# Kernel optimization log

Measured on AMD Instinct MI355X. Metric: run time of the kernel, lower is better.

The kernel has to match this reference:

```python
import jax, jax.numpy as jnp
import numpy as np

N, D, H, O, E, K = 8192, 1024, 4096, 1024, 8, 3  # tokens, in_dim, hidden, out_dim, experts, topk


def setup_inputs() -> dict:
    key = jax.random.key(0)
    ks = jax.random.split(key, 4)
    s = 0.02
    return {
        "x": jax.random.normal(ks[0], (N, D), jnp.float32),
        "gate_w": jax.random.normal(ks[1], (D, E), jnp.float32) * s,
        "gate_b": jnp.zeros((E,), jnp.float32),
        "w1": jax.random.normal(ks[2], (E, D, H), jnp.float32) * s,
        "b1": jnp.zeros((E, H), jnp.float32),
        "w2": jax.random.normal(ks[3], (E, H, O), jnp.float32) * s,
        "b2": jnp.zeros((E, O), jnp.float32),
    }


def reference(x, gate_w, gate_b, w1, b1, w2, b2):
    # Gate: scores over experts, top-k mask, softmax renormalized over selected experts
    scores = x @ gate_w + gate_b                                   # [N, E]
    _, topk_idx = jax.lax.top_k(scores, K)                         # [N, K]
    mask = jax.nn.one_hot(topk_idx, E, dtype=scores.dtype).sum(1)  # [N, E] (topk indices are distinct)
    weights = jax.nn.softmax(scores, axis=-1) * mask
    weights = weights / (weights.sum(-1, keepdims=True) + 1e-8)
    # Dense all-expert MLP (faithful to original: every expert runs on every token)
    h = jax.nn.relu(jnp.einsum('nd,edh->neh', x, w1) + b1)         # [N, E, H]
    outs = jnp.einsum('neh,eho->neo', h, w2) + b2                  # [N, E, O]
    # Weighted combine over experts
    return jnp.einsum('ne,neo->no', weights, outs)                 # [N, O]
```

## Files before the change

kernel.cpp:

```cpp
#include <hip/hip_runtime.h>
#include <hip/hip_bf16.h>
#include <hip/hip_fp16.h>

#define N_TOK 8192
#define DIM_D 1024
#define DIM_H 4096
#define DIM_O 1024
#define NEXP  8
#define TOPK  3

#define CAP_ROWS  25600
#define MAX_TILES 200

typedef _Float16 f16_t;
typedef _Float16 f16x4 __attribute__((ext_vector_type(4)));
typedef _Float16 f16x8 __attribute__((ext_vector_type(8)));
typedef float    floatx4 __attribute__((ext_vector_type(4)));

__device__ __forceinline__ void gld_lds16(const void* g, void* l) {
  __builtin_amdgcn_global_load_lds(
      (__attribute__((address_space(1))) void*)(void*)g,
      (__attribute__((address_space(3))) void*)l, 16, 0, 0);
}

__global__ __launch_bounds__(256) void gate_kernel(
    const float* __restrict__ x, const float* __restrict__ gw,
    const float* __restrict__ gb, float* __restrict__ wts,
    int* __restrict__ lists, int* __restrict__ cnt) {
  const int token = blockIdx.x * 4 + (threadIdx.x >> 6);
  const int lane = threadIdx.x & 63;
  float s[NEXP];
#pragma unroll
  for (int e = 0; e < NEXP; e++) s[e] = 0.f;
  const float* xr = x + (size_t)token * DIM_D;
  for (int d = lane; d < DIM_D; d += 64) {
    const float xv = xr[d];
    const float* g = gw + (size_t)d * NEXP;
#pragma unroll
    for (int e = 0; e < NEXP; e++) s[e] += xv * g[e];
  }
#pragma unroll
  for (int off = 32; off > 0; off >>= 1) {
#pragma unroll
    for (int e = 0; e < NEXP; e++) s[e] += __shfl_xor(s[e], off, 64);
  }
#pragma unroll
  for (int e = 0; e < NEXP; e++) s[e] += gb[e];

  float mx = s[0];
#pragma unroll
  for (int e = 1; e < NEXP; e++) mx = fmaxf(mx, s[e]);
  float p[NEXP];
  float den = 0.f;
#pragma unroll
  for (int e = 0; e < NEXP; e++) { p[e] = expf(s[e] - mx); den += p[e]; }

  bool sel[NEXP];
#pragma unroll
  for (int e = 0; e < NEXP; e++) sel[e] = false;
  for (int k = 0; k < TOPK; k++) {
    int bj = 0;
    float bv = -1e30f;
#pragma unroll
    for (int e = 0; e < NEXP; e++) {
      if (!sel[e] && s[e] > bv) { bv = s[e]; bj = e; }
    }
    sel[bj] = true;
  }
  float msum = 1e-8f * den;
#pragma unroll
  for (int e = 0; e < NEXP; e++) msum += sel[e] ? p[e] : 0.f;
  const float inv = 1.f / msum;
  if (lane < NEXP) {
    wts[(size_t)token * NEXP + lane] = sel[lane] ? p[lane] * inv : 0.f;
  }
  if (lane == 0) {
#pragma unroll
    for (int e = 0; e < NEXP; e++) {
      if (sel[e]) {
        const int pos = atomicAdd(&cnt[e], 1);
        lists[e * N_TOK + pos] = token;
      }
    }
  }
}

__global__ void plan_kernel(const int* __restrict__ cnt, int* __restrict__ start,
                            int* __restrict__ table, int* __restrict__ total) {
  if (threadIdx.x == 0) {
    int r0 = 0, t = 0;
    for (int e = 0; e < NEXP; e++) {
      start[e] = r0;
      const int nt = (cnt[e] + 127) >> 7;
      for (int i = 0; i < nt; i++) table[t++] = (e << 16) | ((r0 >> 7) + i);
      r0 += nt << 7;
    }
    total[0] = t;
  }
}

__global__ __launch_bounds__(256) void fill_kernel(
    const int* __restrict__ cnt, const int* __restrict__ start,
    const int* __restrict__ lists, const float* __restrict__ wts,
    int* __restrict__ rowtok, float* __restrict__ roww) {
  const int e = blockIdx.y;
  const int i = blockIdx.x * 256 + threadIdx.x;
  const int c = cnt[e];
  const int pad = (c + 127) & ~127;
  if (i >= pad) return;
  const int r = start[e] + i;
  if (i < c) {
    const int t = lists[e * N_TOK + i];
    rowtok[r] = t;
    roww[r] = wts[(size_t)t * NEXP + e];
  } else {
    rowtok[r] = -1;
    roww[r] = 0.f;
  }
}

__global__ __launch_bounds__(256) void cvt_f32_f16(
    const float* __restrict__ in, f16_t* __restrict__ out, int n4) {
  const int i = blockIdx.x * 256 + threadIdx.x;
  if (i >= n4) return;
  const float4 v = ((const float4*)in)[i];
  f16x4 o;
  o.x = (f16_t)v.x; o.y = (f16_t)v.y; o.z = (f16_t)v.z; o.w = (f16_t)v.w;
  ((f16x4*)out)[i] = o;
}

__global__ __launch_bounds__(256) void cvt_transpose(
    const float* __restrict__ in, f16_t* __restrict__ out, int R, int C) {
  __shared__ float tile[32][33];
  const int e = blockIdx.z;
  const int r0 = blockIdx.y * 32, c0 = blockIdx.x * 32;
  const int lc = threadIdx.x & 31, lr0 = threadIdx.x >> 5;
  const float* src = in + (size_t)e * R * C;
#pragma unroll
  for (int i = 0; i < 4; i++) {
    const int rr = lr0 + i * 8;
    tile[rr][lc] = src[(size_t)(r0 + rr) * C + c0 + lc];
  }
  __syncthreads();
  f16_t* dst = out + (size_t)e * C * R;
#pragma unroll
  for (int i = 0; i < 4; i++) {
    const int cc = lr0 + i * 8;
    dst[(size_t)(c0 + cc) * R + r0 + lc] = (f16_t)tile[lc][cc];
  }
}

__global__ __launch_bounds__(256, 2) void gemm1_moe(
    const f16_t* __restrict__ xb, const f16_t* __restrict__ w1t,
    const float* __restrict__ b1, const int* __restrict__ rowtok,
    const int* __restrict__ table, const int* __restrict__ total,
    f16_t* __restrict__ hg, int Hc, int cH) {
  const int mt = blockIdx.y;
  if (mt >= total[0]) return;
  const int ent = table[mt];
  const int e = ent >> 16;
  const int r0 = (ent & 0xffff) << 7;
  const int n0 = blockIdx.x * 128;

  __shared__ __align__(16) f16_t Asm[128 * 32];
  __shared__ __align__(16) f16_t Bsm[128 * 32];
  const int tid = threadIdx.x;
  const int wave = tid >> 6, lane = tid & 63;
  const int q = lane >> 4, r = lane & 15;
  const int waveM = (wave >> 1) * 64, waveN = (wave & 1) * 64;

  const floatx4 zero = {0.f, 0.f, 0.f, 0.f};
  floatx4 acc[4][4];
#pragma unroll
  for (int mi = 0; mi < 4; mi++)
#pragma unroll
    for (int ni = 0; ni < 4; ni++) acc[mi][ni] = zero;

  const f16_t* BT = w1t + (size_t)e * DIM_H * DIM_D + (size_t)cH * DIM_D;

  const int s0 = tid, s1 = tid + 256;
  const int row0 = s0 >> 2, row1 = s1 >> 2;
  const int gs0 = (s0 & 3) ^ ((row0 >> 1) & 3);
  const int gs1 = (s1 & 3) ^ ((row1 >> 1) & 3);
  const int tok0 = max(rowtok[r0 + row0], 0);
  const int tok1 = max(rowtok[r0 + row1], 0);
  const f16_t* Ar0 = xb + (size_t)tok0 * DIM_D + gs0 * 8;
  const f16_t* Ar1 = xb + (size_t)tok1 * DIM_D + gs1 * 8;
  const f16_t* Br0 = BT + (size_t)(n0 + row0) * DIM_D + gs0 * 8;
  const f16_t* Br1 = BT + (size_t)(n0 + row1) * DIM_D + gs1 * 8;
  f16_t* AsmB0 = &Asm[(wave * 64) * 8];
  f16_t* AsmB1 = &Asm[(256 + wave * 64) * 8];
  f16_t* BsmB0 = &Bsm[(wave * 64) * 8];
  f16_t* BsmB1 = &Bsm[(256 + wave * 64) * 8];

  for (int k0 = 0; k0 < DIM_D; k0 += 32) {
    gld_lds16(Ar0 + k0, AsmB0);
    gld_lds16(Ar1 + k0, AsmB1);
    gld_lds16(Br0 + k0, BsmB0);
    gld_lds16(Br1 + k0, BsmB1);
    __syncthreads();
    f16x8 af[4], bfr[4];
#pragma unroll
    for (int i = 0; i < 4; i++) {
      const int rowa = waveM + i * 16 + r;
      af[i] = *(const f16x8*)&Asm[rowa * 32 + ((q ^ ((rowa >> 1) & 3)) << 3)];
      const int rowb = waveN + i * 16 + r;
      bfr[i] = *(const f16x8*)&Bsm[rowb * 32 + ((q ^ ((rowb >> 1) & 3)) << 3)];
    }
#pragma unroll
    for (int mi = 0; mi < 4; mi++)
#pragma unroll
      for (int ni = 0; ni < 4; ni++)
        acc[mi][ni] = __builtin_amdgcn_mfma_f32_16x16x32_f16(
            af[mi], bfr[ni], acc[mi][ni], 0, 0, 0);
    __syncthreads();
  }

#pragma unroll
  for (int mi = 0; mi < 4; mi++)
#pragma unroll
    for (int ni = 0; ni < 4; ni++) {
      const int gcol = n0 + waveN + ni * 16 + r;
      const float bv = b1[(size_t)e * DIM_H + cH + gcol];
#pragma unroll
      for (int rr = 0; rr < 4; rr++) {
        const int grow = r0 + waveM + mi * 16 + q * 4 + rr;
        hg[(size_t)grow * Hc + gcol] = (f16_t)fmaxf(acc[mi][ni][rr] + bv, 0.f);
      }
    }
}

__global__ __launch_bounds__(256, 2) void gemm2_moe(
    const f16_t* __restrict__ hg, const f16_t* __restrict__ w2t,
    const float* __restrict__ b2, const int* __restrict__ rowtok,
    const float* __restrict__ roww, const int* __restrict__ table,
    const int* __restrict__ total, float* __restrict__ out, int Hc, int cH,
    int addBias) {
  const int mt = blockIdx.y;
  if (mt >= total[0]) return;
  const int ent = table[mt];
  const int e = ent >> 16;
  const int r0 = (ent & 0xffff) << 7;
  const int n0 = blockIdx.x * 128;

  __shared__ __align__(16) f16_t Asm[128 * 32];
  __shared__ __align__(16) f16_t Bsm[128 * 32];
  const int tid = threadIdx.x;
  const int wave = tid >> 6, lane = tid & 63;
  const int q = lane >> 4, r = lane & 15;
  const int waveM = (wave >> 1) * 64, waveN = (wave & 1) * 64;

  const floatx4 zero = {0.f, 0.f, 0.f, 0.f};
  floatx4 acc[4][4];
#pragma unroll
  for (int mi = 0; mi < 4; mi++)
#pragma unroll
    for (int ni = 0; ni < 4; ni++) acc[mi][ni] = zero;

  const f16_t* BT = w2t + (size_t)e * DIM_O * DIM_H + cH;

  const int s0 = tid, s1 = tid + 256;
  const int row0 = s0 >> 2, row1 = s1 >> 2;
  const int gs0 = (s0 & 3) ^ ((row0 >> 1) & 3);
  const int gs1 = (s1 & 3) ^ ((row1 >> 1) & 3);
  const f16_t* Ar0 = hg + (size_t)(r0 + row0) * Hc + gs0 * 8;
  const f16_t* Ar1 = hg + (size_t)(r0 + row1) * Hc + gs1 * 8;
  const f16_t* Br0 = BT + (size_t)(n0 + row0) * DIM_H + gs0 * 8;
  const f16_t* Br1 = BT + (size_t)(n0 + row1) * DIM_H + gs1 * 8;
  f16_t* AsmB0 = &Asm[(wave * 64) * 8];
  f16_t* AsmB1 = &Asm[(256 + wave * 64) * 8];
  f16_t* BsmB0 = &Bsm[(wave * 64) * 8];
  f16_t* BsmB1 = &Bsm[(256 + wave * 64) * 8];

  for (int k0 = 0; k0 < Hc; k0 += 32) {
    gld_lds16(Ar0 + k0, AsmB0);
    gld_lds16(Ar1 + k0, AsmB1);
    gld_lds16(Br0 + k0, BsmB0);
    gld_lds16(Br1 + k0, BsmB1);
    __syncthreads();
    f16x8 af[4], bfr[4];
#pragma unroll
    for (int i = 0; i < 4; i++) {
      const int rowa = waveM + i * 16 + r;
      af[i] = *(const f16x8*)&Asm[rowa * 32 + ((q ^ ((rowa >> 1) & 3)) << 3)];
      const int rowb = waveN + i * 16 + r;
      bfr[i] = *(const f16x8*)&Bsm[rowb * 32 + ((q ^ ((rowb >> 1) & 3)) << 3)];
    }
#pragma unroll
    for (int mi = 0; mi < 4; mi++)
#pragma unroll
      for (int ni = 0; ni < 4; ni++)
        acc[mi][ni] = __builtin_amdgcn_mfma_f32_16x16x32_f16(
            af[mi], bfr[ni], acc[mi][ni], 0, 0, 0);
    __syncthreads();
  }

#pragma unroll
  for (int mi = 0; mi < 4; mi++)
#pragma unroll
    for (int ni = 0; ni < 4; ni++) {
      const int gcol = n0 + waveN + ni * 16 + r;
      const float bv = addBias ? b2[(size_t)e * DIM_O + gcol] : 0.f;
#pragma unroll
      for (int rr = 0; rr < 4; rr++) {
        const int grow = r0 + waveM + mi * 16 + q * 4 + rr;
        const int t = rowtok[grow];
        if (t >= 0) {
          const float w = roww[grow];
          unsafeAtomicAdd(&out[(size_t)t * DIM_O + gcol],
                          w * (acc[mi][ni][rr] + bv));
        }
      }
    }
}

extern "C" void kernel_launch(void* const* d_in, const int* in_sizes, int n_in,
                              void* d_out, int out_size, void* d_ws, size_t ws_size,
                              hipStream_t stream) {
  const float* x      = (const float*)d_in[0];
  const float* gate_w = (const float*)d_in[1];
  const float* gate_b = (const float*)d_in[2];
  const float* w1     = (const float*)d_in[3];
  const float* b1     = (const float*)d_in[4];
  const float* w2     = (const float*)d_in[5];
  const float* b2     = (const float*)d_in[6];
  float* out = (float*)d_out;

  char* ws = (char*)d_ws;
  const size_t off_wts    = 0;
  const size_t off_lists  = off_wts + 262144;
  const size_t off_cnt    = off_lists + 262144;
  const size_t off_start  = off_cnt + 512;
  const size_t off_total  = off_start + 512;
  const size_t off_table  = off_total + 512;
  const size_t off_rowtok = off_table + 2048;
  const size_t off_roww   = off_rowtok + 102400;
  const size_t META       = 1 << 20;
  const size_t off_w1t = META;
  const size_t off_w2t = off_w1t + (size_t)NEXP * DIM_H * DIM_D * 2;
  const size_t off_xb  = off_w2t + (size_t)NEXP * DIM_O * DIM_H * 2;
  const size_t off_hg  = off_xb + (size_t)N_TOK * DIM_D * 2;

  float* wts   = (float*)(ws + off_wts);
  int*   lists = (int*)(ws + off_lists);
  int*   cnt   = (int*)(ws + off_cnt);
  int*   start = (int*)(ws + off_start);
  int*   total = (int*)(ws + off_total);
  int*   table = (int*)(ws + off_table);
  int*   rowtok= (int*)(ws + off_rowtok);
  float* roww  = (float*)(ws + off_roww);
  f16_t* w1t   = (f16_t*)(ws + off_w1t);
  f16_t* w2t   = (f16_t*)(ws + off_w2t);
  f16_t* xb    = (f16_t*)(ws + off_xb);
  f16_t* hg    = (f16_t*)(ws + off_hg);

  int Hc = 512;
  for (int cand = 4096; cand >= 512; cand >>= 1) {
    if (off_hg + (size_t)CAP_ROWS * cand * 2 <= ws_size) { Hc = cand; break; }
  }
  const int nchunks = DIM_H / Hc;

  hipMemsetAsync(cnt, 0, 512, stream);
  hipMemsetAsync(d_out, 0, (size_t)out_size * sizeof(float), stream);

  gate_kernel<<<N_TOK / 4, 256, 0, stream>>>(x, gate_w, gate_b, wts, lists, cnt);
  plan_kernel<<<1, 64, 0, stream>>>(cnt, start, table, total);
  fill_kernel<<<dim3(N_TOK / 256, NEXP), 256, 0, stream>>>(
      cnt, start, lists, wts, rowtok, roww);

  const int n4 = N_TOK * DIM_D / 4;
  cvt_f32_f16<<<(n4 + 255) / 256, 256, 0, stream>>>(x, xb, n4);
  cvt_transpose<<<dim3(DIM_H / 32, DIM_D / 32, NEXP), 256, 0, stream>>>(
      w1, w1t, DIM_D, DIM_H);
  cvt_transpose<<<dim3(DIM_O / 32, DIM_H / 32, NEXP), 256, 0, stream>>>(
      w2, w2t, DIM_H, DIM_O);

  for (int c = 0; c < nchunks; c++) {
    const int cH = c * Hc;
    gemm1_moe<<<dim3(Hc / 128, MAX_TILES), 256, 0, stream>>>(
        xb, w1t, b1, rowtok, table, total, hg, Hc, cH);
    gemm2_moe<<<dim3(DIM_O / 128, MAX_TILES), 256, 0, stream>>>(
        hg, w2t, b2, rowtok, roww, table, total, out, Hc, cH, c == 0);
  }
}
```

Measured before the change: 1.284 ms.

## Enlarge MoE GEMM row tiles to 256 and parallelize tile table construction

The grouped GEMM kernels now process 256-row tiles instead of 128, with each wave owning a 128x64 sub-tile and holding 8x4 MFMA accumulators. This doubles reuse of each B-operand load per LDS stage and halves the tile count. Expert row padding, capacity and workspace offsets are adjusted to match, and the plan kernel fills the tile table across threads. The larger tiles raise register pressure, which can lower occupancy, and add more padding waste per expert.

```diff
diff --git a/kernel.cpp b/kernel.cpp
--- a/kernel.cpp
+++ b/kernel.cpp
@@ -9,8 +9,8 @@
 #define NEXP  8
 #define TOPK  3
 
-#define CAP_ROWS  25600
-#define MAX_TILES 200
+#define CAP_ROWS  26624
+#define MAX_TILES 104
 
 typedef _Float16 f16_t;
 typedef _Float16 f16x4 __attribute__((ext_vector_type(4)));
@@ -85,17 +85,29 @@
   }
 }
 
-__global__ void plan_kernel(const int* __restrict__ cnt, int* __restrict__ start,
-                            int* __restrict__ table, int* __restrict__ total) {
+__global__ __launch_bounds__(256) void plan_kernel(
+    const int* __restrict__ cnt, int* __restrict__ start,
+    int* __restrict__ table, int* __restrict__ total) {
+  __shared__ int s_start[NEXP], s_tp[NEXP + 1];
   if (threadIdx.x == 0) {
     int r0 = 0, t = 0;
     for (int e = 0; e < NEXP; e++) {
-      start[e] = r0;
-      const int nt = (cnt[e] + 127) >> 7;
-      for (int i = 0; i < nt; i++) table[t++] = (e << 16) | ((r0 >> 7) + i);
-      r0 += nt << 7;
-    }
+      s_start[e] = r0;
+      s_tp[e] = t;
+      const int nt = (cnt[e] + 255) >> 8;
+      t += nt;
+      r0 += nt << 8;
+      start[e] = s_start[e];
+    }
+    s_tp[NEXP] = t;
     total[0] = t;
+  }
+  __syncthreads();
+  const int t = threadIdx.x;
+  if (t < s_tp[NEXP]) {
+    int e = 0;
+    while (t >= s_tp[e + 1]) e++;
+    table[t] = (e << 16) | ((s_start[e] >> 8) + (t - s_tp[e]));
   }
 }
 
@@ -106,7 +118,7 @@
   const int e = blockIdx.y;
   const int i = blockIdx.x * 256 + threadIdx.x;
   const int c = cnt[e];
-  const int pad = (c + 127) & ~127;
+  const int pad = (c + 255) & ~255;
   if (i >= pad) return;
   const int r = start[e] + i;
   if (i < c) {
@@ -159,56 +171,66 @@
   if (mt >= total[0]) return;
   const int ent = table[mt];
   const int e = ent >> 16;
-  const int r0 = (ent & 0xffff) << 7;
+  const int r0 = (ent & 0xffff) << 8;
   const int n0 = blockIdx.x * 128;
 
-  __shared__ __align__(16) f16_t Asm[128 * 32];
+  __shared__ __align__(16) f16_t Asm[256 * 32];
   __shared__ __align__(16) f16_t Bsm[128 * 32];
   const int tid = threadIdx.x;
   const int wave = tid >> 6, lane = tid & 63;
   const int q = lane >> 4, r = lane & 15;
-  const int waveM = (wave >> 1) * 64, waveN = (wave & 1) * 64;
+  const int waveM = (wave >> 1) * 128, waveN = (wave & 1) * 64;
 
   const floatx4 zero = {0.f, 0.f, 0.f, 0.f};
-  floatx4 acc[4][4];
-#pragma unroll
-  for (int mi = 0; mi < 4; mi++)
+  floatx4 acc[8][4];
+#pragma unroll
+  for (int mi = 0; mi < 8; mi++)
 #pragma unroll
     for (int ni = 0; ni < 4; ni++) acc[mi][ni] = zero;
 
   const f16_t* BT = w1t + (size_t)e * DIM_H * DIM_D + (size_t)cH * DIM_D;
 
-  const int s0 = tid, s1 = tid + 256;
-  const int row0 = s0 >> 2, row1 = s1 >> 2;
-  const int gs0 = (s0 & 3) ^ ((row0 >> 1) & 3);
-  const int gs1 = (s1 & 3) ^ ((row1 >> 1) & 3);
-  const int tok0 = max(rowtok[r0 + row0], 0);
-  const int tok1 = max(rowtok[r0 + row1], 0);
-  const f16_t* Ar0 = xb + (size_t)tok0 * DIM_D + gs0 * 8;
-  const f16_t* Ar1 = xb + (size_t)tok1 * DIM_D + gs1 * 8;
-  const f16_t* Br0 = BT + (size_t)(n0 + row0) * DIM_D + gs0 * 8;
-  const f16_t* Br1 = BT + (size_t)(n0 + row1) * DIM_D + gs1 * 8;
-  f16_t* AsmB0 = &Asm[(wave * 64) * 8];
-  f16_t* AsmB1 = &Asm[(256 + wave * 64) * 8];
-  f16_t* BsmB0 = &Bsm[(wave * 64) * 8];
-  f16_t* BsmB1 = &Bsm[(256 + wave * 64) * 8];
+  const f16_t* Asrc[4];
+  f16_t* AsmB[4];
+#pragma unroll
+  for (int j = 0; j < 4; j++) {
+    const int s = tid + j * 256;
+    const int row = s >> 2;
+    const int gs = (s & 3) ^ ((row >> 1) & 3);
+    const int tok = max(rowtok[r0 + row], 0);
+    Asrc[j] = xb + (size_t)tok * DIM_D + gs * 8;
+    AsmB[j] = &Asm[(wave * 64 + j * 256) * 8];
+  }
+  const f16_t* Bsrc[2];
+  f16_t* BsmB[2];
+#pragma unroll
+  for (int j = 0; j < 2; j++) {
+    const int s = tid + j * 256;
+    const int row = s >> 2;
+    const int gs = (s & 3) ^ ((row >> 1) & 3);
+    Bsrc[j] = BT + (size_t)(n0 + row) * DIM_D + gs * 8;
+    BsmB[j] = &Bsm[(wave * 64 + j * 256) * 8];
+  }
 
   for (int k0 = 0; k0 < DIM_D; k0 += 32) {
-    gld_lds16(Ar0 + k0, AsmB0);
-    gld_lds16(Ar1 + k0, AsmB1);
-    gld_lds16(Br0 + k0, BsmB0);
-    gld_lds16(Br1 + k0, BsmB1);
+#pragma unroll
+    for (int j = 0; j < 4; j++) gld_lds16(Asrc[j] + k0, AsmB[j]);
+#pragma unroll
+    for (int j = 0; j < 2; j++) gld_lds16(Bsrc[j] + k0, BsmB[j]);
     __syncthreads();
-    f16x8 af[4], bfr[4];
-#pragma unroll
-    for (int i = 0; i < 4; i++) {
+    f16x8 af[8], bfr[4];
+#pragma unroll
+    for (int i = 0; i < 8; i++) {
       const int rowa = waveM + i * 16 + r;
       af[i] = *(const f16x8*)&Asm[rowa * 32 + ((q ^ ((rowa >> 1) & 3)) << 3)];
+    }
+#pragma unroll
+    for (int i = 0; i < 4; i++) {
       const int rowb = waveN + i * 16 + r;
       bfr[i] = *(const f16x8*)&Bsm[rowb * 32 + ((q ^ ((rowb >> 1) & 3)) << 3)];
     }
 #pragma unroll
-    for (int mi = 0; mi < 4; mi++)
+    for (int mi = 0; mi < 8; mi++)
 #pragma unroll
       for (int ni = 0; ni < 4; ni++)
         acc[mi][ni] = __builtin_amdgcn_mfma_f32_16x16x32_f16(
@@ -217,7 +239,7 @@
   }
 
 #pragma unroll
-  for (int mi = 0; mi < 4; mi++)
+  for (int mi = 0; mi < 8; mi++)
 #pragma unroll
     for (int ni = 0; ni < 4; ni++) {
       const int gcol = n0 + waveN + ni * 16 + r;
@@ -240,54 +262,65 @@
   if (mt >= total[0]) return;
   const int ent = table[mt];
   const int e = ent >> 16;
-  const int r0 = (ent & 0xffff) << 7;
+  const int r0 = (ent & 0xffff) << 8;
   const int n0 = blockIdx.x * 128;
 
-  __shared__ __align__(16) f16_t Asm[128 * 32];
+  __shared__ __align__(16) f16_t Asm[256 * 32];
   __shared__ __align__(16) f16_t Bsm[128 * 32];
   const int tid = threadIdx.x;
   const int wave = tid >> 6, lane = tid & 63;
   const int q = lane >> 4, r = lane & 15;
-  const int waveM = (wave >> 1) * 64, waveN = (wave & 1) * 64;
+  const int waveM = (wave >> 1) * 128, waveN = (wave & 1) * 64;
 
   const floatx4 zero = {0.f, 0.f, 0.f, 0.f};
-  floatx4 acc[4][4];
-#pragma unroll
-  for (int mi = 0; mi < 4; mi++)
+  floatx4 acc[8][4];
+#pragma unroll
+  for (int mi = 0; mi < 8; mi++)
 #pragma unroll
     for (int ni = 0; ni < 4; ni++) acc[mi][ni] = zero;
 
   const f16_t* BT = w2t + (size_t)e * DIM_O * DIM_H + cH;
 
-  const int s0 = tid, s1 = tid + 256;
-  const int row0 = s0 >> 2, row1 = s1 >> 2;
-  const int gs0 = (s0 & 3) ^ ((row0 >> 1) & 3);
-  const int gs1 = (s1 & 3) ^ ((row1 >> 1) & 3);
-  const f16_t* Ar0 = hg + (size_t)(r0 + row0) * Hc + gs0 * 8;
-  const f16_t* Ar1 = hg + (size_t)(r0 + row1) * Hc + gs1 * 8;
-  const f16_t* Br0 = BT + (size_t)(n0 + row0) * DIM_H + gs0 * 8;
-  const f16_t* Br1 = BT + (size_t)(n0 + row1) * DIM_H + gs1 * 8;
-  f16_t* AsmB0 = &Asm[(wave * 64) * 8];
-  f16_t* AsmB1 = &Asm[(256 + wave * 64) * 8];
-  f16_t* BsmB0 = &Bsm[(wave * 64) * 8];
-  f16_t* BsmB1 = &Bsm[(256 + wave * 64) * 8];
+  const f16_t* Asrc[4];
+  f16_t* AsmB[4];
+#pragma unroll
+  for (int j = 0; j < 4; j++) {
+    const int s = tid + j * 256;
+    const int row = s >> 2;
+    const int gs = (s & 3) ^ ((row >> 1) & 3);
+    Asrc[j] = hg + (size_t)(r0 + row) * Hc + gs * 8;
+    AsmB[j] = &Asm[(wave * 64 + j * 256) * 8];
+  }
+  const f16_t* Bsrc[2];
+  f16_t* BsmB[2];
+#pragma unroll
+  for (int j = 0; j < 2; j++) {
+    const int s = tid + j * 256;
+    const int row = s >> 2;
+    const int gs = (s & 3) ^ ((row >> 1) & 3);
+    Bsrc[j] = BT + (size_t)(n0 + row) * DIM_H + gs * 8;
+    BsmB[j] = &Bsm[(wave * 64 + j * 256) * 8];
+  }
 
   for (int k0 = 0; k0 < Hc; k0 += 32) {
-    gld_lds16(Ar0 + k0, AsmB0);
-    gld_lds16(Ar1 + k0, AsmB1);
-    gld_lds16(Br0 + k0, BsmB0);
-    gld_lds16(Br1 + k0, BsmB1);
+#pragma unroll
+    for (int j = 0; j < 4; j++) gld_lds16(Asrc[j] + k0, AsmB[j]);
+#pragma unroll
+    for (int j = 0; j < 2; j++) gld_lds16(Bsrc[j] + k0, BsmB[j]);
     __syncthreads();
-    f16x8 af[4], bfr[4];
-#pragma unroll
-    for (int i = 0; i < 4; i++) {
+    f16x8 af[8], bfr[4];
+#pragma unroll
+    for (int i = 0; i < 8; i++) {
       const int rowa = waveM + i * 16 + r;
       af[i] = *(const f16x8*)&Asm[rowa * 32 + ((q ^ ((rowa >> 1) & 3)) << 3)];
+    }
+#pragma unroll
+    for (int i = 0; i < 4; i++) {
       const int rowb = waveN + i * 16 + r;
       bfr[i] = *(const f16x8*)&Bsm[rowb * 32 + ((q ^ ((rowb >> 1) & 3)) << 3)];
     }
 #pragma unroll
-    for (int mi = 0; mi < 4; mi++)
+    for (int mi = 0; mi < 8; mi++)
 #pragma unroll
       for (int ni = 0; ni < 4; ni++)
         acc[mi][ni] = __builtin_amdgcn_mfma_f32_16x16x32_f16(
@@ -296,7 +329,7 @@
   }
 
 #pragma unroll
-  for (int mi = 0; mi < 4; mi++)
+  for (int mi = 0; mi < 8; mi++)
 #pragma unroll
     for (int ni = 0; ni < 4; ni++) {
       const int gcol = n0 + waveN + ni * 16 + r;
@@ -328,13 +361,13 @@
 
   char* ws = (char*)d_ws;
   const size_t off_wts    = 0;
-  const size_t off_lists  = off_wts + 262144;
-  const size_t off_cnt    = off_lists + 262144;
-  const size_t off_start  = off_cnt + 512;
-  const size_t off_total  = off_start + 512;
-  const size_t off_table  = off_total + 512;
-  const size_t off_rowtok = off_table + 2048;
-  const size_t off_roww   = off_rowtok + 102400;
+  const size_t off_lists  = 0x40000;
+  const size_t off_cnt    = 0x80000;
+  const size_t off_start  = 0x80200;
+  const size_t off_total  = 0x80400;
+  const size_t off_table  = 0x80600;
+  const size_t off_rowtok = 0x90000;
+  const size_t off_roww   = 0xB0000;
   const size_t META       = 1 << 20;
   const size_t off_w1t = META;
   const size_t off_w2t = off_w1t + (size_t)NEXP * DIM_H * DIM_D * 2;
@@ -364,7 +397,7 @@
   hipMemsetAsync(d_out, 0, (size_t)out_size * sizeof(float), stream);
 
   gate_kernel<<<N_TOK / 4, 256, 0, stream>>>(x, gate_w, gate_b, wts, lists, cnt);
-  plan_kernel<<<1, 64, 0, stream>>>(cnt, start, table, total);
+  plan_kernel<<<1, 256, 0, stream>>>(cnt, start, table, total);
   fill_kernel<<<dim3(N_TOK / 256, NEXP), 256, 0, stream>>>(
       cnt, start, lists, wts, rowtok, roww);
 
```

Measured after the change: 1.482 ms. 1.15x slower.
